# Kernel tuning notes

Hardware: AMD Instinct MI355X
Metric: run time of the kernel (lower is better)

The kernel has to match this reference:

```python
import jax, jax.numpy as jnp
import numpy as np

K = 1024      # codebook_size
D = 64        # embedding_dim
DECAY = 0.99
EPS = 1e-05


def setup_inputs() -> dict:
    key = jax.random.key(0)
    k1, k2, k3 = jax.random.split(key, 3)
    z_e = jax.random.normal(k1, (16, D, 64, 64), dtype=jnp.float32)
    emb = jax.random.normal(k2, (D, K), dtype=jnp.float32) * 0.05
    emb_ema = emb  # buffer initialized as clone of emb
    counts_ema = jnp.zeros((K,), dtype=jnp.float32)
    return {"z_e": z_e, "emb": emb, "emb_ema": emb_ema, "counts_ema": counts_ema}


def reference(z_e, emb, emb_ema, counts_ema):
    B, Dd, H, W = z_e.shape
    # [B,D,H,W] -> [B*H*W, D]
    z = jnp.transpose(z_e, (0, 2, 3, 1)).reshape(-1, Dd)
    # squared L2 distance to each code: [N, K]
    dist = (z * z).sum(1, keepdims=True) - 2.0 * (z @ emb) + (emb * emb).sum(0, keepdims=True)
    idx = jnp.argmin(dist, axis=1)                      # [N]
    embeddings = emb.T[idx]                             # [N, D]
    z_q = z + jax.lax.stop_gradient(embeddings - z)     # straight-through

    # EMA codebook update (no_grad in original)
    zg = jax.lax.stop_gradient(z)
    counts = jnp.zeros((K,), dtype=emb.dtype).at[idx].add(1.0)          # one-hot column sums
    counts_ema_new = counts_ema + (1.0 - DECAY) * (counts - counts_ema)
    emb_update = jax.ops.segment_sum(zg, idx, num_segments=K).T          # [D, K]
    emb_ema_new = emb_ema + (1.0 - DECAY) * (emb_update - emb_ema)
    n = counts_ema_new.sum()
    counts_norm = (counts_ema_new + EPS) / (n + K * EPS) * n
    emb_new = emb_ema_new / counts_norm[None, :]

    z_q_out = jnp.transpose(z_q.reshape(B, H, W, Dd), (0, 3, 1, 2))      # back to [B,D,H,W]
    idx_out = idx.reshape(B, H, W)
    return z_q_out, idx_out, emb_new, emb_ema_new, counts_ema_new
```

## Files before the change

### kernel.cpp

```cpp
#include <hip/hip_runtime.h>
#include <math.h>

#define KCODES 1024
#define DDIM   64
#define NCOPY  4

constexpr size_t O_ZQ  = 0;
constexpr size_t O_IDX = 4194304;
constexpr size_t O_EMB = O_IDX + 65536;
constexpr size_t O_EMA = O_EMB + 65536;
constexpr size_t O_CEN = O_EMA + 65536;

constexpr size_t W_UPD   = 0;
constexpr size_t W_CNT   = 262144;
constexpr size_t W_ENORM = 266240;
constexpr size_t W_EN2   = 267264;
constexpr size_t W_EMAXA = 268288;
constexpr size_t W_FLAGN = 268304;
constexpr size_t W_FLAGL = 268320;
constexpr int    FLAGCAP = 8192;
constexpr size_t W_EMBT  = 276512;
constexpr size_t W_G16H  = 342048;
constexpr size_t W_G16L  = 374816;

typedef _Float16 f16;
typedef f16 f16x8 __attribute__((ext_vector_type(8)));
typedef float f32x4 __attribute__((ext_vector_type(4)));

#define MF(a, b, c) __builtin_amdgcn_mfma_f32_16x16x32_f16((a), (b), (c), 0, 0, 0)

static __device__ __forceinline__ void gload16(const void* g, void* l) {
  __builtin_amdgcn_global_load_lds(
      (const __attribute__((address_space(1))) void*)g,
      (__attribute__((address_space(3))) void*)l, 16, 0, 0);
}

__global__ __launch_bounds__(256) void vq_prep(const float* __restrict__ emb,
                                               float* __restrict__ ws) {
  __shared__ float t_lds[64 * 65];
  const int tid = threadIdx.x;
  const int g   = blockIdx.x;

  if (g < 16) {
    const int k0 = g * 64;
    #pragma unroll
    for (int it = 0; it < 16; ++it) {
      const int idx = tid + it * 256;
      const int d   = idx >> 6;
      const int kq  = idx & 63;
      t_lds[d * 65 + kq] = emb[d * KCODES + k0 + kq];
    }
    __syncthreads();

    f16* gh = (f16*)(ws + W_G16H);
    f16* gl = (f16*)(ws + W_G16L);
    #pragma unroll
    for (int it = 0; it < 16; ++it) {
      const int idx = tid + it * 256;
      const int kk  = idx >> 6;
      const int d   = idx & 63;
      const float v = t_lds[d * 65 + kk];
      ws[W_EMBT + (size_t)(k0 + kk) * 64 + d] = v;
      const f16 hi = (f16)v;
      const f16 lo = (f16)(v - (float)hi);
      const int u  = (d >> 3) ^ (kk & 7);
      const size_t fo = (size_t)g * 4096 + kk * 64 + u * 8 + (d & 7);
      gh[fo] = hi;
      gl[fo] = lo;
    }

    if (tid < 64) {
      const int k = tid;
      float s = 0.f;
      #pragma unroll
      for (int d = 0; d < DDIM; ++d) {
        const float v = t_lds[d * 65 + k];
        s = fmaf(v, v, s);
      }
      ws[W_ENORM + k0 + k] = s;
      ws[W_EN2   + k0 + k] = -0.5f * s;
      float mx = s;
      #pragma unroll
      for (int off = 1; off < 64; off <<= 1) mx = fmaxf(mx, __shfl_xor(mx, off, 64));
      if (tid == 0) ws[W_EMAXA + g] = mx;
    }
  }

  {
    float4* base = (float4*)(ws + W_UPD);
    const int total4 = 66560;
    for (int idx = g * 256 + tid; idx < total4; idx += 64 * 256)
      base[idx] = float4{0.f, 0.f, 0.f, 0.f};
  }
  if (g == 0 && tid == 0) ((int*)(ws + W_FLAGN))[0] = 0;
}

#define ZP 132
__global__ __launch_bounds__(256, 2) void vq_main(
    const float* __restrict__ z_e,
    const float* __restrict__ g16h,
    const float* __restrict__ g16l,
    const float* __restrict__ embT,
    const float* __restrict__ en2,
    const float* __restrict__ emaxa,
    float* __restrict__ upd,
    float* __restrict__ cnt,
    int*   __restrict__ flagn,
    int*   __restrict__ flagl,
    float* __restrict__ out) {
  __shared__ float z_lds[DDIM * ZP];
  __shared__ __align__(16) f16 e_hi[2][4096];
  __shared__ __align__(16) f16 e_lo[2][4096];
  __shared__ __align__(16) float en2_lds[KCODES];
  __shared__ int bidx[128];

  const int tid  = threadIdx.x;
  const int bid  = blockIdx.x;
  const int wv   = tid >> 6;
  const int lane = tid & 63;
  const int m    = lane & 15;
  const int q    = lane >> 4;
  const int r0   = wv * 32 + m;
  const int r1   = r0 + 16;

  float* updc = upd + ((size_t)(bid & (NCOPY - 1)) << 16);
  float* cntc = cnt + ((size_t)(bid & (NCOPY - 1)) << 10);

  const int n0  = bid * 128;
  const int b   = n0 >> 12;
  const int hw0 = n0 & 4095;
  const size_t zbase = (size_t)b * 262144 + (size_t)hw0;

  {
    const char* sh = (const char*)g16h + (size_t)(wv * 2) * 1024 + lane * 16;
    const char* sl = (const char*)g16l + (size_t)(wv * 2) * 1024 + lane * 16;
    char* dh = (char*)&e_hi[0][0] + (wv * 2) * 1024;
    char* dl = (char*)&e_lo[0][0] + (wv * 2) * 1024;
    gload16(sh, dh);           gload16(sh + 1024, dh + 1024);
    gload16(sl, dl);           gload16(sl + 1024, dl + 1024);
  }

  {
    const float4* z4 = (const float4*)(z_e + zbase);
    #pragma unroll
    for (int it = 0; it < 8; ++it) {
      const int f  = tid + it * 256;
      const int d  = f >> 5;
      const int r4 = f & 31;
      const float4 v = z4[(size_t)d * 1024 + r4];
      *(float4*)(z_lds + d * ZP + r4 * 4) = v;
    }
  }
  ((float4*)en2_lds)[tid] = ((const float4*)en2)[tid];

  float emax = 0.f;
  {
    const float4* e4 = (const float4*)emaxa;
    #pragma unroll
    for (int i = 0; i < 4; ++i) {
      const float4 v = e4[i];
      emax = fmaxf(emax, fmaxf(fmaxf(v.x, v.y), fmaxf(v.z, v.w)));
    }
  }
  __syncthreads();

  f16x8 b0h_0, b1h_0, b0l_0, b1l_0, b0h_1, b1h_1, b0l_1, b1l_1;
  float zz0 = 0.f, zz1 = 0.f;
  #pragma unroll
  for (int j = 0; j < 8; ++j) {
    const int d0 = q * 8 + j, d1 = 32 + q * 8 + j;
    const float v00 = z_lds[d0 * ZP + r0];
    const float v01 = z_lds[d1 * ZP + r0];
    const float v10 = z_lds[d0 * ZP + r1];
    const float v11 = z_lds[d1 * ZP + r1];
    zz0 = fmaf(v00, v00, zz0); zz0 = fmaf(v01, v01, zz0);
    zz1 = fmaf(v10, v10, zz1); zz1 = fmaf(v11, v11, zz1);
    const f16 h00 = (f16)v00, h01 = (f16)v01, h10 = (f16)v10, h11 = (f16)v11;
    b0h_0[j] = h00; b1h_0[j] = h01; b0h_1[j] = h10; b1h_1[j] = h11;
    b0l_0[j] = (f16)(v00 - (float)h00);
    b1l_0[j] = (f16)(v01 - (float)h01);
    b0l_1[j] = (f16)(v10 - (float)h10);
    b1l_1[j] = (f16)(v11 - (float)h11);
  }
  zz0 += __shfl_xor(zz0, 16, 64); zz0 += __shfl_xor(zz0, 32, 64);
  zz1 += __shfl_xor(zz1, 16, 64); zz1 += __shfl_xor(zz1, 32, 64);

  const int lcl7  = m & 7;
  const int aoff0 = m * 128 + ((q)     ^ lcl7) * 16;
  const int aoff1 = m * 128 + ((4 + q) ^ lcl7) * 16;

  float M1_0 = -INFINITY, M2_0 = -INFINITY, M1_1 = -INFINITY, M2_1 = -INFINITY;
  int   I1_0 = 0, I1_1 = 0;

  #pragma unroll 1
  for (int c = 0; c < 16; ++c) {
    const int cb = c & 1;
    if (c < 15) {
      const int nb = cb ^ 1;
      const size_t so = (size_t)(c + 1) * 8192 + (wv * 2) * 1024 + lane * 16;
      const char* sh = (const char*)g16h + so;
      const char* sl = (const char*)g16l + so;
      char* dh = (char*)&e_hi[nb][0] + (wv * 2) * 1024;
      char* dl = (char*)&e_lo[nb][0] + (wv * 2) * 1024;
      gload16(sh, dh);           gload16(sh + 1024, dh + 1024);
      gload16(sl, dl);           gload16(sl + 1024, dl + 1024);
    }
    const char* eb = (const char*)&e_hi[cb][0];
    const char* lb = (const char*)&e_lo[cb][0];
    __builtin_amdgcn_s_setprio(1);
    #pragma unroll
    for (int t = 0; t < 4; ++t) {
      const f16x8 a0h = *(const f16x8*)(eb + t * 2048 + aoff0);
      const f16x8 a1h = *(const f16x8*)(eb + t * 2048 + aoff1);
      const f16x8 a0l = *(const f16x8*)(lb + t * 2048 + aoff0);
      const f16x8 a1l = *(const f16x8*)(lb + t * 2048 + aoff1);
      const f32x4 en2f = *(const f32x4*)(en2_lds + c * 64 + t * 16 + q * 4);
      f32x4 acc0 = en2f, acc1 = en2f;
      acc0 = MF(a0l, b0h_0, acc0);  acc1 = MF(a0l, b0h_1, acc1);
      acc0 = MF(a1l, b1h_0, acc0);  acc1 = MF(a1l, b1h_1, acc1);
      acc0 = MF(a0h, b0l_0, acc0);  acc1 = MF(a0h, b0l_1, acc1);
      acc0 = MF(a1h, b1l_0, acc0);  acc1 = MF(a1h, b1l_1, acc1);
      acc0 = MF(a0h, b0h_0, acc0);  acc1 = MF(a0h, b0h_1, acc1);
      acc0 = MF(a1h, b1h_0, acc0);  acc1 = MF(a1h, b1h_1, acc1);
      const int ib = c * 64 + t * 16 + q * 4;
      #pragma unroll
      for (int r = 0; r < 4; ++r) {
        const float a = acc0[r];
        const bool gt = a > M1_0;
        M2_0 = fmaxf(M2_0, fminf(a, M1_0));
        if (gt) I1_0 = ib + r;
        M1_0 = fmaxf(M1_0, a);
        const float a1v = acc1[r];
        const bool gt1 = a1v > M1_1;
        M2_1 = fmaxf(M2_1, fminf(a1v, M1_1));
        if (gt1) I1_1 = ib + r;
        M1_1 = fmaxf(M1_1, a1v);
      }
    }
    __builtin_amdgcn_s_setprio(0);
    __syncthreads();
  }

  #pragma unroll
  for (int off = 16; off <= 32; off <<= 1) {
    {
      const float o1 = __shfl_xor(M1_0, off, 64);
      const float o2 = __shfl_xor(M2_0, off, 64);
      const int   oi = __shfl_xor(I1_0, off, 64);
      const float nm2 = fmaxf(fmaxf(M2_0, o2), fminf(M1_0, o1));
      if (o1 > M1_0) I1_0 = oi;
      M1_0 = fmaxf(M1_0, o1);
      M2_0 = nm2;
    }
    {
      const float o1 = __shfl_xor(M1_1, off, 64);
      const float o2 = __shfl_xor(M2_1, off, 64);
      const int   oi = __shfl_xor(I1_1, off, 64);
      const float nm2 = fmaxf(fmaxf(M2_1, o2), fminf(M1_1, o1));
      if (o1 > M1_1) I1_1 = oi;
      M1_1 = fmaxf(M1_1, o1);
      M2_1 = nm2;
    }
  }

  if (lane < 32) {
    const int s   = lane >> 4;
    const int row = wv * 32 + s * 16 + m;
    const float MM1 = s ? M1_1 : M1_0;
    const float MM2 = s ? M2_1 : M2_0;
    const int   II  = s ? I1_1 : I1_0;
    const float zzv = s ? zz1 : zz0;
    const float Mh = 5.0e-5f * sqrtf(zzv * emax);
    if (MM1 - MM2 > Mh) {
      bidx[row] = II;
      out[O_IDX + n0 + row] = (float)II;
      atomicAdd(cntc + II, 1.0f);
    } else {
      bidx[row] = -1;
      const int sl = atomicAdd(flagn, 1);
      if (sl < FLAGCAP) flagl[sl] = n0 + row;
    }
  }
  __syncthreads();

  {
    const int row  = tid & 127;
    const int half = tid >> 7;
    const int code = bidx[row];
    if (code >= 0) {
      const float4* er4 = (const float4*)(embT + (size_t)code * 64);
      #pragma unroll
      for (int qq = 0; qq < 8; ++qq) {
        const float4 e4 = er4[half * 8 + qq];
        const float ev[4] = {e4.x, e4.y, e4.z, e4.w};
        #pragma unroll
        for (int x = 0; x < 4; ++x) {
          const int d = half * 32 + qq * 4 + x;
          const float zv = z_lds[d * ZP + row];
          out[O_ZQ + zbase + (size_t)d * 4096 + row] = zv + (ev[x] - zv);
        }
      }
    }
  }

  {
    #pragma unroll 4
    for (int rr = 0; rr < 32; ++rr) {
      const int row  = wv * 32 + rr;
      const int code = bidx[row];
      if (code >= 0)
        atomicAdd(updc + (size_t)code * 64 + lane, z_lds[lane * ZP + row]);
    }
  }
}

__global__ __launch_bounds__(256) void vq_rescore(
    const float* __restrict__ z_e,
    const float* __restrict__ embT,
    const float* __restrict__ eN,
    const int* __restrict__ flagn,
    const int* __restrict__ flagl,
    float* __restrict__ upd,
    float* __restrict__ cnt,
    float* __restrict__ out) {
  __shared__ float zrow[64];
  __shared__ float wv_v[4];
  __shared__ int   wv_i[4];
  __shared__ int   bestc;

  const int tid = threadIdx.x;
  int nf = *flagn;
  if (nf > FLAGCAP) nf = FLAGCAP;

  for (int j = blockIdx.x; j < nf; j += gridDim.x) {
    __syncthreads();
    const int rowid = flagl[j];
    const int bb = rowid >> 12;
    const int hw = rowid & 4095;
    const size_t base = (size_t)bb * 262144 + (size_t)hw;
    if (tid < 64) zrow[tid] = z_e[base + (size_t)tid * 4096];
    __syncthreads();

    float bm = INFINITY;
    int   bi = 0;
    #pragma unroll
    for (int cc = 0; cc < 4; ++cc) {
      const int k = tid * 4 + cc;
      const float4* e4p = (const float4*)(embT + (size_t)k * 64);
      float a0 = 0.f, a1 = 0.f, a2 = 0.f, a3 = 0.f;
      #pragma unroll
      for (int d4 = 0; d4 < 16; ++d4) {
        const float4 e4 = e4p[d4];
        a0 = fmaf(zrow[d4 * 4 + 0], e4.x, a0);
        a1 = fmaf(zrow[d4 * 4 + 1], e4.y, a1);
        a2 = fmaf(zrow[d4 * 4 + 2], e4.z, a2);
        a3 = fmaf(zrow[d4 * 4 + 3], e4.w, a3);
      }
      const float dist = fmaf(-2.f, (a0 + a1) + (a2 + a3), eN[k]);
      if (dist < bm) { bm = dist; bi = k; }
    }
    #pragma unroll
    for (int mm = 1; mm < 64; mm <<= 1) {
      const float v2 = __shfl_xor(bm, mm, 64);
      const int   i2 = __shfl_xor(bi, mm, 64);
      if (v2 < bm || (v2 == bm && i2 < bi)) { bm = v2; bi = i2; }
    }
    if ((tid & 63) == 0) { wv_v[tid >> 6] = bm; wv_i[tid >> 6] = bi; }
    __syncthreads();
    if (tid == 0) {
      float v = wv_v[0]; int ix = wv_i[0];
      #pragma unroll
      for (int w = 1; w < 4; ++w) {
        if (wv_v[w] < v || (wv_v[w] == v && wv_i[w] < ix)) { v = wv_v[w]; ix = wv_i[w]; }
      }
      bestc = ix;
      out[O_IDX + rowid] = (float)ix;
      atomicAdd(cnt + ix, 1.0f);
    }
    __syncthreads();
    if (tid < 64) {
      const int d = tid;
      const float zv = zrow[d];
      const float ev = embT[(size_t)bestc * 64 + d];
      out[O_ZQ + base + (size_t)d * 4096] = zv + (ev - zv);
      atomicAdd(upd + (size_t)bestc * 64 + d, zv);
    }
  }
}

__global__ __launch_bounds__(256) void vq_final(const float* __restrict__ emb_ema,
                                                const float* __restrict__ counts_ema,
                                                const float* __restrict__ ws,
                                                float* __restrict__ out) {
  __shared__ float red[256];
  const int tid = threadIdx.x;
  const float* cnt = ws + W_CNT;
  const float* upd = ws + W_UPD;

  float psum = 0.f;
  for (int t = tid; t < KCODES; t += 256) {
    float c = 0.f;
    #pragma unroll
    for (int p = 0; p < NCOPY; ++p) c += cnt[p * KCODES + t];
    const float ce  = counts_ema[t];
    const float cen = ce + 0.01f * (c - ce);
    psum += cen;
    if (blockIdx.x == 0) out[O_CEN + t] = cen;
  }
  red[tid] = psum;
  __syncthreads();
  #pragma unroll
  for (int s = 128; s > 0; s >>= 1) {
    if (tid < s) red[tid] += red[tid + s];
    __syncthreads();
  }
  const float nsum = red[0];

  const int i = blockIdx.x * 256 + tid;
  const int d = i >> 10;
  const int k = i & 1023;

  float c = 0.f;
  #pragma unroll
  for (int p = 0; p < NCOPY; ++p) c += cnt[p * KCODES + k];
  const float ce  = counts_ema[k];
  const float cen = ce + 0.01f * (c - ce);
  const float norm = (cen + 1e-5f) / (nsum + (float)KCODES * 1e-5f) * nsum;

  float us = 0.f;
  #pragma unroll
  for (int p = 0; p < NCOPY; ++p) us += upd[(size_t)p * 65536 + (size_t)k * 64 + d];
  const float ema     = emb_ema[i];
  const float ema_new = ema + 0.01f * (us - ema);
  out[O_EMA + i] = ema_new;
  out[O_EMB + i] = ema_new / norm;
}

extern "C" void kernel_launch(void* const* d_in, const int* in_sizes, int n_in,
                              void* d_out, int out_size, void* d_ws, size_t ws_size,
                              hipStream_t stream) {
  const float* z_e        = (const float*)d_in[0];
  const float* emb        = (const float*)d_in[1];
  const float* emb_ema    = (const float*)d_in[2];
  const float* counts_ema = (const float*)d_in[3];
  float* out = (float*)d_out;
  float* ws  = (float*)d_ws;

  vq_prep<<<64, 256, 0, stream>>>(emb, ws);
  vq_main<<<512, 256, 0, stream>>>(z_e, ws + W_G16H, ws + W_G16L,
                                   ws + W_EMBT, ws + W_EN2, ws + W_EMAXA,
                                   ws + W_UPD, ws + W_CNT,
                                   (int*)(ws + W_FLAGN), (int*)(ws + W_FLAGL), out);
  vq_rescore<<<256, 256, 0, stream>>>(z_e, ws + W_EMBT, ws + W_ENORM,
                                      (int*)(ws + W_FLAGN), (int*)(ws + W_FLAGL),
                                      ws + W_UPD, ws + W_CNT, out);
  vq_final<<<256, 256, 0, stream>>>(emb_ema, counts_ema, ws, out);
}
```

Measured before the change: 138.0 us.

## Fuse ambiguous-row exact rescoring into main VQ kernel, drop rescore launch

Rows whose fp16 top-two margin is too small are no longer written to a global flag list for a separate rescoring kernel. Each block now keeps them in a shared-memory list and rescores them in fp32 right after its main pass, reading z from the LDS tile it already holds. This removes one kernel launch, the global flag counter and list, and the reload of z rows from global memory. In exchange the rescore work sits on each block's tail, which can leave blocks with many flagged rows as stragglers. The old 8192-row global cap is also gone.

```diff
diff --git a/kernel.cpp b/kernel.cpp
--- a/kernel.cpp
+++ b/kernel.cpp
@@ -16,9 +16,6 @@
 constexpr size_t W_ENORM = 266240;
 constexpr size_t W_EN2   = 267264;
 constexpr size_t W_EMAXA = 268288;
-constexpr size_t W_FLAGN = 268304;
-constexpr size_t W_FLAGL = 268320;
-constexpr int    FLAGCAP = 8192;
 constexpr size_t W_EMBT  = 276512;
 constexpr size_t W_G16H  = 342048;
 constexpr size_t W_G16L  = 374816;
@@ -92,7 +89,6 @@
     for (int idx = g * 256 + tid; idx < total4; idx += 64 * 256)
       base[idx] = float4{0.f, 0.f, 0.f, 0.f};
   }
-  if (g == 0 && tid == 0) ((int*)(ws + W_FLAGN))[0] = 0;
 }
 
 #define ZP 132
@@ -101,18 +97,22 @@
     const float* __restrict__ g16h,
     const float* __restrict__ g16l,
     const float* __restrict__ embT,
+    const float* __restrict__ eN,
     const float* __restrict__ en2,
     const float* __restrict__ emaxa,
     float* __restrict__ upd,
     float* __restrict__ cnt,
-    int*   __restrict__ flagn,
-    int*   __restrict__ flagl,
     float* __restrict__ out) {
   __shared__ float z_lds[DDIM * ZP];
   __shared__ __align__(16) f16 e_hi[2][4096];
   __shared__ __align__(16) f16 e_lo[2][4096];
   __shared__ __align__(16) float en2_lds[KCODES];
-  __shared__ int bidx[128];
+  __shared__ int   bidx[128];
+  __shared__ int   flr[128];
+  __shared__ int   flc;
+  __shared__ float wv_v[4];
+  __shared__ int   wv_i[4];
+  __shared__ int   bestc;
 
   const int tid  = threadIdx.x;
   const int bid  = blockIdx.x;
@@ -130,6 +130,8 @@
   const int b   = n0 >> 12;
   const int hw0 = n0 & 4095;
   const size_t zbase = (size_t)b * 262144 + (size_t)hw0;
+
+  if (tid == 0) flc = 0;
 
   {
     const char* sh = (const char*)g16h + (size_t)(wv * 2) * 1024 + lane * 16;
@@ -277,8 +279,8 @@
       atomicAdd(cntc + II, 1.0f);
     } else {
       bidx[row] = -1;
-      const int sl = atomicAdd(flagn, 1);
-      if (sl < FLAGCAP) flagl[sl] = n0 + row;
+      const int sl = atomicAdd(&flc, 1);
+      flr[sl] = row;
     }
   }
   __syncthreads();
@@ -312,35 +314,10 @@
         atomicAdd(updc + (size_t)code * 64 + lane, z_lds[lane * ZP + row]);
     }
   }
-}
-
-__global__ __launch_bounds__(256) void vq_rescore(
-    const float* __restrict__ z_e,
-    const float* __restrict__ embT,
-    const float* __restrict__ eN,
-    const int* __restrict__ flagn,
-    const int* __restrict__ flagl,
-    float* __restrict__ upd,
-    float* __restrict__ cnt,
-    float* __restrict__ out) {
-  __shared__ float zrow[64];
-  __shared__ float wv_v[4];
-  __shared__ int   wv_i[4];
-  __shared__ int   bestc;
-
-  const int tid = threadIdx.x;
-  int nf = *flagn;
-  if (nf > FLAGCAP) nf = FLAGCAP;
-
-  for (int j = blockIdx.x; j < nf; j += gridDim.x) {
-    __syncthreads();
-    const int rowid = flagl[j];
-    const int bb = rowid >> 12;
-    const int hw = rowid & 4095;
-    const size_t base = (size_t)bb * 262144 + (size_t)hw;
-    if (tid < 64) zrow[tid] = z_e[base + (size_t)tid * 4096];
-    __syncthreads();
-
+
+  const int nfl = flc;
+  for (int j = 0; j < nfl; ++j) {
+    const int row = flr[j];
     float bm = INFINITY;
     int   bi = 0;
     #pragma unroll
@@ -351,10 +328,10 @@
       #pragma unroll
       for (int d4 = 0; d4 < 16; ++d4) {
         const float4 e4 = e4p[d4];
-        a0 = fmaf(zrow[d4 * 4 + 0], e4.x, a0);
-        a1 = fmaf(zrow[d4 * 4 + 1], e4.y, a1);
-        a2 = fmaf(zrow[d4 * 4 + 2], e4.z, a2);
-        a3 = fmaf(zrow[d4 * 4 + 3], e4.w, a3);
+        a0 = fmaf(z_lds[(d4 * 4 + 0) * ZP + row], e4.x, a0);
+        a1 = fmaf(z_lds[(d4 * 4 + 1) * ZP + row], e4.y, a1);
+        a2 = fmaf(z_lds[(d4 * 4 + 2) * ZP + row], e4.z, a2);
+        a3 = fmaf(z_lds[(d4 * 4 + 3) * ZP + row], e4.w, a3);
       }
       const float dist = fmaf(-2.f, (a0 + a1) + (a2 + a3), eN[k]);
       if (dist < bm) { bm = dist; bi = k; }
@@ -365,7 +342,7 @@
       const int   i2 = __shfl_xor(bi, mm, 64);
       if (v2 < bm || (v2 == bm && i2 < bi)) { bm = v2; bi = i2; }
     }
-    if ((tid & 63) == 0) { wv_v[tid >> 6] = bm; wv_i[tid >> 6] = bi; }
+    if (lane == 0) { wv_v[wv] = bm; wv_i[wv] = bi; }
     __syncthreads();
     if (tid == 0) {
       float v = wv_v[0]; int ix = wv_i[0];
@@ -374,16 +351,17 @@
         if (wv_v[w] < v || (wv_v[w] == v && wv_i[w] < ix)) { v = wv_v[w]; ix = wv_i[w]; }
       }
       bestc = ix;
-      out[O_IDX + rowid] = (float)ix;
-      atomicAdd(cnt + ix, 1.0f);
+      out[O_IDX + n0 + row] = (float)ix;
+      atomicAdd(cntc + ix, 1.0f);
     }
     __syncthreads();
+    const int code = bestc;
     if (tid < 64) {
       const int d = tid;
-      const float zv = zrow[d];
-      const float ev = embT[(size_t)bestc * 64 + d];
-      out[O_ZQ + base + (size_t)d * 4096] = zv + (ev - zv);
-      atomicAdd(upd + (size_t)bestc * 64 + d, zv);
+      const float zv = z_lds[d * ZP + row];
+      const float ev = embT[(size_t)code * 64 + d];
+      out[O_ZQ + zbase + (size_t)d * 4096 + row] = zv + (ev - zv);
+      atomicAdd(updc + (size_t)code * 64 + d, zv);
     }
   }
 }
@@ -448,11 +426,7 @@
 
   vq_prep<<<64, 256, 0, stream>>>(emb, ws);
   vq_main<<<512, 256, 0, stream>>>(z_e, ws + W_G16H, ws + W_G16L,
-                                   ws + W_EMBT, ws + W_EN2, ws + W_EMAXA,
-                                   ws + W_UPD, ws + W_CNT,
-                                   (int*)(ws + W_FLAGN), (int*)(ws + W_FLAGL), out);
-  vq_rescore<<<256, 256, 0, stream>>>(z_e, ws + W_EMBT, ws + W_ENORM,
-                                      (int*)(ws + W_FLAGN), (int*)(ws + W_FLAGL),
-                                      ws + W_UPD, ws + W_CNT, out);
+                                   ws + W_EMBT, ws + W_ENORM, ws + W_EN2,
+                                   ws + W_EMAXA, ws + W_UPD, ws + W_CNT, out);
   vq_final<<<256, 256, 0, stream>>>(emb_ema, counts_ema, ws, out);
 }
```

New measurement: 162.6 us. 1.18x slower.
